# Optimization experiments

Hardware: AMD Instinct MI355X
Metric: run time of the kernel (lower is better)

Reference implementation:

```python
import jax, jax.numpy as jnp
import numpy as np


def setup_inputs() -> dict:
    key = jax.random.key(0)
    k1, k2 = jax.random.split(key)
    pred = jax.random.normal(k1, (128, 1024), dtype=jnp.float32)
    y = jax.random.normal(k2, (128, 1024), dtype=jnp.float32)
    return {"pred": pred, "y": y}


def reference(pred, y):
    # Original: transpose to [N, C], then per-column soft Kendall tau.
    p = pred.T  # [N, C]
    l = y.T     # [N, C]
    n = p.shape[0]
    # Pairwise outer differences, batched across all C columns at once: [N, N, C]
    diff = p[:, None, :] - p[None, :, :]
    sgn = jnp.sign(l[:, None, :] - l[None, :, :])
    tmp = jnp.tanh(diff * sgn)
    # Diagonal entries are tanh(0) = 0, so subtracting the eye-masked diagonal
    # (as in the original) is a no-op; just sum everything.
    per_col = jnp.sum(tmp, axis=(0, 1)) / (n * (n - 1))  # [C]
    return 1.0 - per_col.mean()
```

## Files before the change

### kernel.cpp

```cpp
#include <hip/hip_runtime.h>


typedef float v2f __attribute__((ext_vector_type(2)));

#define TAU_N 1024
#define TAU_C 128
#define TILE  128
#define NTILE (TAU_N / TILE)
#define NTP   (NTILE * (NTILE + 1) / 2)
#define BPC   4
#define JOBS  (NTP / BPC)
#define PBLK  (TAU_C * BPC)
#define THR   1024
#define IT    4

__device__ __constant__ unsigned char c_TI[NTP] = {
    0,1,1,2,2,2,3,3,3,3,4,4,4,4,4,5,5,5,5,5,5,
    6,6,6,6,6,6,6,7,7,7,7,7,7,7,7};
__device__ __constant__ unsigned char c_TJ[NTP] = {
    0,0,1,0,1,2,0,1,2,3,0,1,2,3,4,0,1,2,3,4,5,
    0,1,2,3,4,5,6,0,1,2,3,4,5,6,7};
__device__ __constant__ float c_W[NTP] = {
    0.5f,1,0.5f,1,1,0.5f,1,1,1,0.5f,1,1,1,1,0.5f,1,1,1,1,1,0.5f,
    1,1,1,1,1,1,0.5f,1,1,1,1,1,1,1,0.5f};

__device__ __forceinline__ v2f tau_group(v2f m2, v2f mly, v2f t2, v2f l2, v2f acc) {
    const v2f one2 = {1.f, 1.f};
    v2f n  = m2 - t2;
    v2f d  = __builtin_elementwise_fma(-m2, t2, one2);
    v2f r  = {__builtin_amdgcn_rcpf(d.x), __builtin_amdgcn_rcpf(d.y)};
    v2f ld = mly - l2;
    v2f ns = {__uint_as_float(__float_as_uint(n.x) ^
                              (__float_as_uint(ld.x) & 0x80000000u)),
              __uint_as_float(__float_as_uint(n.y) ^
                              (__float_as_uint(ld.y) & 0x80000000u))};
    return __builtin_elementwise_fma(ns, r, acc);
}

__global__ __launch_bounds__(THR, 8) void tau_tri_kernel(
        const float* __restrict__ pred, const float* __restrict__ y,
        float* __restrict__ partials) {
    __shared__ __align__(16) float ts[TAU_N];
    __shared__ __align__(16) float ys[TAU_N];
    __shared__ float wsum[THR / 64];

    const int bx  = blockIdx.x;
    const int tid = threadIdx.x;
    const int c   = bx >> 2;
    const int jb0 = (bx & (BPC - 1)) * JOBS;

    const float* p = pred + c * TAU_N;
    const float* l = y    + c * TAU_N;

    ts[tid] = tanhf(p[tid]);
    ys[tid] = l[tid];
    __syncthreads();

    const float4* t4 = (const float4*)ts;
    const float4* y4 = (const float4*)ys;
    const int ig = tid >> 5;
    const int js = tid & 31;

    float acc_tot = 0.f;

#pragma unroll
    for (int q = 0; q < JOBS; ++q) {
        const int job = jb0 + q;
        const int ti  = c_TI[job];
        const int tj  = c_TJ[job];
        const float w = c_W[job];

        const float4 mt4 = t4[ti * (TILE / 4) + ig];
        const float4 ml4 = y4[ti * (TILE / 4) + ig];
        const float4 tj4 = t4[tj * (TILE / 4) + js];
        const float4 yj4 = y4[tj * (TILE / 4) + js];

        const v2f tA = {tj4.x, tj4.y}, tB = {tj4.z, tj4.w};
        const v2f lA = {yj4.x, yj4.y}, lB = {yj4.z, yj4.w};
        const float mt[IT] = {mt4.x, mt4.y, mt4.z, mt4.w};
        const float ml[IT] = {ml4.x, ml4.y, ml4.z, ml4.w};

        v2f a0 = {0.f,0.f}, a1 = {0.f,0.f}, a2 = {0.f,0.f}, a3 = {0.f,0.f};
#pragma unroll
        for (int a = 0; a < IT; ++a) {
            const v2f m2  = {mt[a], mt[a]};
            const v2f mly = {ml[a], ml[a]};
            if (a & 1) {
                a1 = tau_group(m2, mly, tA, lA, a1);
                a3 = tau_group(m2, mly, tB, lB, a3);
            } else {
                a0 = tau_group(m2, mly, tA, lA, a0);
                a2 = tau_group(m2, mly, tB, lB, a2);
            }
        }
        const v2f asum = (a0 + a1) + (a2 + a3);
        acc_tot = __builtin_fmaf(w, asum.x + asum.y, acc_tot);
    }

    for (int off = 32; off >= 1; off >>= 1)
        acc_tot += __shfl_down(acc_tot, off, 64);
    if ((tid & 63) == 0) wsum[tid >> 6] = acc_tot;
    __syncthreads();
    if (tid == 0) {
        float t = 0.f;
#pragma unroll
        for (int w = 0; w < THR / 64; ++w) t += wsum[w];
        partials[bx] = t;
    }
}

__global__ __launch_bounds__(PBLK) void tau_finalize_kernel(
        const float* __restrict__ partials, float* __restrict__ out) {
    __shared__ float wsum[PBLK / 64];
    const int tid = threadIdx.x;
    float acc = partials[tid];
    for (int off = 32; off >= 1; off >>= 1)
        acc += __shfl_down(acc, off, 64);
    if ((tid & 63) == 0) wsum[tid >> 6] = acc;
    __syncthreads();
    if (tid == 0) {
        float t = 0.f;
#pragma unroll
        for (int w = 0; w < PBLK / 64; ++w) t += wsum[w];
        const float scale = 2.0f / ((float)TAU_N * (float)(TAU_N - 1) * (float)TAU_C);
        out[0] = 1.0f - t * scale;
    }
}

extern "C" void kernel_launch(void* const* d_in, const int* in_sizes, int n_in,
                              void* d_out, int out_size, void* d_ws, size_t ws_size,
                              hipStream_t stream) {
    const float* pred = (const float*)d_in[0];
    const float* y    = (const float*)d_in[1];
    float* out        = (float*)d_out;
    float* partials   = (float*)d_ws;

    tau_tri_kernel<<<PBLK, THR, 0, stream>>>(pred, y, partials);
    tau_finalize_kernel<<<1, PBLK, 0, stream>>>(partials, out);
}
```

Measured before the change: 69.84 us.

## Use 8x4 per-thread register tiles with 512 threads and prefetch next job

Halves the block size to 512 threads and has each thread process 8 i-rows against 4 j-columns per tile job, up from 4, doubling register reuse of the row values. Tile-pair jobs are split six ways per column instead of four, and the LDS reads for the next job are software-prefetched into registers while the current job computes. The aim is fewer LDS loads per pairwise tanh term and more latency hiding, at the cost of higher register pressure and a non-power-of-two block-to-column mapping.

Result: no change. 69.01 us (-1.2%).

```diff
diff --git a/kernel.cpp b/kernel.cpp
--- a/kernel.cpp
+++ b/kernel.cpp
@@ -8,11 +8,11 @@
 #define TILE  128
 #define NTILE (TAU_N / TILE)
 #define NTP   (NTILE * (NTILE + 1) / 2)
-#define BPC   4
+#define BPC   6
 #define JOBS  (NTP / BPC)
 #define PBLK  (TAU_C * BPC)
-#define THR   1024
-#define IT    4
+#define THR   512
+#define IT    8
 
 __device__ __constant__ unsigned char c_TI[NTP] = {
     0,1,1,2,2,2,3,3,3,3,4,4,4,4,4,5,5,5,5,5,5,
@@ -37,7 +37,7 @@
     return __builtin_elementwise_fma(ns, r, acc);
 }
 
-__global__ __launch_bounds__(THR, 8) void tau_tri_kernel(
+__global__ __launch_bounds__(THR, 6) void tau_tri_kernel(
         const float* __restrict__ pred, const float* __restrict__ y,
         float* __restrict__ partials) {
     __shared__ __align__(16) float ts[TAU_N];
@@ -46,14 +46,16 @@
 
     const int bx  = blockIdx.x;
     const int tid = threadIdx.x;
-    const int c   = bx >> 2;
-    const int jb0 = (bx & (BPC - 1)) * JOBS;
+    const int c   = bx / BPC;
+    const int jb0 = (bx % BPC) * JOBS;
 
     const float* p = pred + c * TAU_N;
     const float* l = y    + c * TAU_N;
 
-    ts[tid] = tanhf(p[tid]);
-    ys[tid] = l[tid];
+    ts[tid]       = tanhf(p[tid]);
+    ts[tid + THR] = tanhf(p[tid + THR]);
+    ys[tid]       = l[tid];
+    ys[tid + THR] = l[tid + THR];
     __syncthreads();
 
     const float4* t4 = (const float4*)ts;
@@ -61,24 +63,37 @@
     const int ig = tid >> 5;
     const int js = tid & 31;
 
+    float4 ta, tb, la, lb, tj4, yj4;
+    {
+        const int ti0 = c_TI[jb0], tj0 = c_TJ[jb0];
+        const int ib4 = (ti0 * TILE + ig * IT) >> 2;
+        const int jb4 = (tj0 * TILE + js * 4) >> 2;
+        ta = t4[ib4]; tb = t4[ib4 + 1];
+        la = y4[ib4]; lb = y4[ib4 + 1];
+        tj4 = t4[jb4]; yj4 = y4[jb4];
+    }
+
     float acc_tot = 0.f;
 
 #pragma unroll
     for (int q = 0; q < JOBS; ++q) {
-        const int job = jb0 + q;
-        const int ti  = c_TI[job];
-        const int tj  = c_TJ[job];
-        const float w = c_W[job];
+        const float w = c_W[jb0 + q];
+        const float4 cta = ta, ctb = tb, cla = la, clb = lb;
+        const float4 ctj = tj4, cyj = yj4;
 
-        const float4 mt4 = t4[ti * (TILE / 4) + ig];
-        const float4 ml4 = y4[ti * (TILE / 4) + ig];
-        const float4 tj4 = t4[tj * (TILE / 4) + js];
-        const float4 yj4 = y4[tj * (TILE / 4) + js];
+        if (q + 1 < JOBS) {
+            const int tin = c_TI[jb0 + q + 1], tjn = c_TJ[jb0 + q + 1];
+            const int ib4 = (tin * TILE + ig * IT) >> 2;
+            const int jb4 = (tjn * TILE + js * 4) >> 2;
+            ta = t4[ib4]; tb = t4[ib4 + 1];
+            la = y4[ib4]; lb = y4[ib4 + 1];
+            tj4 = t4[jb4]; yj4 = y4[jb4];
+        }
 
-        const v2f tA = {tj4.x, tj4.y}, tB = {tj4.z, tj4.w};
-        const v2f lA = {yj4.x, yj4.y}, lB = {yj4.z, yj4.w};
-        const float mt[IT] = {mt4.x, mt4.y, mt4.z, mt4.w};
-        const float ml[IT] = {ml4.x, ml4.y, ml4.z, ml4.w};
+        const v2f tA = {ctj.x, ctj.y}, tB = {ctj.z, ctj.w};
+        const v2f lA = {cyj.x, cyj.y}, lB = {cyj.z, cyj.w};
+        const float mt[IT] = {cta.x, cta.y, cta.z, cta.w, ctb.x, ctb.y, ctb.z, ctb.w};
+        const float ml[IT] = {cla.x, cla.y, cla.z, cla.w, clb.x, clb.y, clb.z, clb.w};
 
         v2f a0 = {0.f,0.f}, a1 = {0.f,0.f}, a2 = {0.f,0.f}, a3 = {0.f,0.f};
 #pragma unroll
```
